# Optimization experiments

Measured on AMD Instinct MI355X. Metric: run time of the kernel, lower is better.

## Reference

```python
import jax, jax.numpy as jnp
import numpy as np

SEQ, BATCH, INP = 20, 16384, 2
HID, EMB = 256, 64
TARGET_LEN = 30


def setup_inputs() -> dict:
    key = jax.random.key(0)
    ks = jax.random.split(key, 12)
    s = 0.1
    return {
        "x_input": jax.random.normal(ks[0], (SEQ, BATCH, INP), dtype=jnp.float32),
        # encoder embedding Linear(input_size -> emb_dim)
        "W_emb": jax.random.normal(ks[1], (EMB, INP), dtype=jnp.float32) * s,
        "b_emb": jax.random.normal(ks[2], (EMB,), dtype=jnp.float32) * s,
        # encoder LSTM (input EMB -> hidden HID), PyTorch gate order i,f,g,o; bias = b_ih + b_hh
        "W_ih_enc": jax.random.normal(ks[3], (4 * HID, EMB), dtype=jnp.float32) * s,
        "W_hh_enc": jax.random.normal(ks[4], (4 * HID, HID), dtype=jnp.float32) * s,
        "b_enc": jax.random.normal(ks[5], (4 * HID,), dtype=jnp.float32) * s,
        # decoder LSTM (input INP -> hidden HID)
        "W_ih_dec": jax.random.normal(ks[6], (4 * HID, INP), dtype=jnp.float32) * s,
        "W_hh_dec": jax.random.normal(ks[7], (4 * HID, HID), dtype=jnp.float32) * s,
        "b_dec": jax.random.normal(ks[8], (4 * HID,), dtype=jnp.float32) * s,
        # decoder output Linear(hidden -> input_size)
        "W_out": jax.random.normal(ks[9], (INP, HID), dtype=jnp.float32) * s,
        "b_out": jax.random.normal(ks[10], (INP,), dtype=jnp.float32) * s,
        "target_len": TARGET_LEN,
    }


def _lstm_cell(x, h, c, W_ih, W_hh, b):
    # x: [B, in], h/c: [B, H]; PyTorch gate order: input, forget, cell(g), output
    gates = x @ W_ih.T + h @ W_hh.T + b  # [B, 4H]
    i, f, g, o = jnp.split(gates, 4, axis=-1)
    c_new = jax.nn.sigmoid(f) * c + jax.nn.sigmoid(i) * jnp.tanh(g)
    h_new = jax.nn.sigmoid(o) * jnp.tanh(c_new)
    return h_new, c_new


def reference(x_input, W_emb, b_emb, W_ih_enc, W_hh_enc, b_enc,
              W_ih_dec, W_hh_dec, b_dec, W_out, b_out, target_len):
    B = x_input.shape[1]
    # --- encoder ---
    x_emb = x_input @ W_emb.T + b_emb  # [S, B, EMB]
    h0 = jnp.zeros((B, HID), dtype=x_input.dtype)
    c0 = jnp.zeros((B, HID), dtype=x_input.dtype)

    def enc_step(carry, xt):
        h, c = carry
        h, c = _lstm_cell(xt, h, c, W_ih_enc, W_hh_enc, b_enc)
        return (h, c), None

    (h_enc, c_enc), _ = jax.lax.scan(enc_step, (h0, c0), x_emb)

    dec_in0 = x_input[-1]  # [B, INP]

    def dec_step(carry, _):
        di, h, c = carry
        h, c = _lstm_cell(di, h, c, W_ih_dec, W_hh_dec, b_dec)
        out = h @ W_out.T + b_out  # [B, INP]
        return (out, h, c), out

    _, outputs = jax.lax.scan(dec_step, (dec_in0, h_enc, c_enc), None,
                              length=int(target_len))
    return outputs  # [target_len, B, INP]
```

## Files before the change

kernel.cpp:

```cpp
#include <hip/hip_runtime.h>


#define SEQ  20
#define TLEN 30

typedef _Float16 half8   __attribute__((ext_vector_type(8)));
typedef _Float16 half4   __attribute__((ext_vector_type(4)));
typedef float    floatx4 __attribute__((ext_vector_type(4)));

__device__ _Float16 g_w_enc[1024 * 288];
__device__ _Float16 g_w_dec0[1024 * 288];
__device__ _Float16 g_w_deff[1024 * 288];
__device__ _Float16 g_wout[512];

__global__ void prep_kernel(const float* __restrict__ W_emb,
                            const float* __restrict__ b_emb,
                            const float* __restrict__ W_ih_enc,
                            const float* __restrict__ W_hh_enc,
                            const float* __restrict__ b_enc,
                            const float* __restrict__ W_ih_dec,
                            const float* __restrict__ W_hh_dec,
                            const float* __restrict__ b_dec,
                            const float* __restrict__ W_out,
                            const float* __restrict__ b_out) {
    int gid = blockIdx.x * blockDim.x + threadIdx.x;
    int stride = gridDim.x * blockDim.x;
    for (int s = gid; s < 1024 * 288; s += stride) {
        int n = s / 288, k = s - n * 288;
        int g = n >> 8, c = (n >> 4) & 15, l16 = n & 15;
        int w = c >> 1, cc = c & 1;
        int i = cc * 4 + g;
        int kt = k >> 5, q = (k >> 3) & 3, j = k & 7;
        int dst = ((w * 9 + kt) * 8 + i) * 512 + q * 128 + l16 * 8 + j;
        float fe = 0.f, fd = 0.f, ff = 0.f;
        if (k < 256) {
            fe = W_hh_enc[n * 256 + k];
            fd = W_hh_dec[n * 256 + k];
            ff = fd + W_ih_dec[2 * n] * W_out[k]
                    + W_ih_dec[2 * n + 1] * W_out[256 + k];
        } else {
            int kp = k - 256;
            if (kp < 2) {
                fd = W_ih_dec[2 * n + kp];
                const float* wr = &W_ih_enc[n * 64];
                for (int e = 0; e < 64; e++) fe = fmaf(wr[e], W_emb[2 * e + kp], fe);
            } else if (kp == 2) {
                fd = b_dec[n];
                ff = b_dec[n] + W_ih_dec[2 * n] * b_out[0]
                              + W_ih_dec[2 * n + 1] * b_out[1];
                fe = b_enc[n];
                const float* wr = &W_ih_enc[n * 64];
                for (int e = 0; e < 64; e++) fe = fmaf(wr[e], b_emb[e], fe);
            }
        }
        g_w_enc[dst]  = (_Float16)fe;
        g_w_dec0[dst] = (_Float16)fd;
        g_w_deff[dst] = (_Float16)ff;
    }
    if (gid < 512) g_wout[gid] = (_Float16)W_out[gid];
}

__global__ __launch_bounds__(512, 2) void lstm_fused(
        const float* __restrict__ x_input,
        const float* __restrict__ b_out,
        float* __restrict__ out)
{
    __shared__ __align__(16) _Float16 h_pack[2][18432];
    __shared__ __align__(16) float    partial_lds[2][8 * 132];

    const int tid = threadIdx.x;
    const int w   = tid >> 6;
    const int L   = tid & 63;
    const int l16 = L & 15;
    const int q   = L >> 4;
    const long row0 = (long)blockIdx.x * 64;

    {
        int* hz = (int*)&h_pack[0][0];
        for (int idx = tid; idx < 18432; idx += 512) hz[idx] = 0;
    }
    __syncthreads();
    if (tid < 128) {
        int buf = tid >> 6, b = tid & 63;
        h_pack[buf][((b >> 4) * 9 + 8) * 512 + (b & 15) * 8 + 2] = (_Float16)1.f;
    }
    if (tid < 128) {
        int b = tid >> 1, jj = tid & 1;
        h_pack[0][((b >> 4) * 9 + 8) * 512 + (b & 15) * 8 + jj] =
            (_Float16)x_input[(row0 + b) * 2 + jj];
    }

    const float bo = b_out[tid & 1];
    const int aoff = q * 128 + l16 * 8;
    const _Float16* __restrict__ wenc_w  = &g_w_enc[w * 36864];
    const _Float16* __restrict__ wdec0_w = &g_w_dec0[w * 36864];
    const _Float16* __restrict__ wdeff_w = &g_w_deff[w * 36864];

    _Float16 wo[2][2][4];
#pragma unroll
    for (int jj = 0; jj < 2; jj++)
#pragma unroll
        for (int cc = 0; cc < 2; cc++)
#pragma unroll
            for (int r = 0; r < 4; r++)
                wo[jj][cc][r] = g_wout[jj * 256 + 32 * w + 16 * cc + 4 * q + r];

    floatx4 acc[8][4];
    float   c_st[4][2][4];
#pragma unroll
    for (int nt = 0; nt < 4; nt++)
#pragma unroll
        for (int cc = 0; cc < 2; cc++)
#pragma unroll
            for (int r = 0; r < 4; r++) c_st[nt][cc][r] = 0.f;

    __syncthreads();

    int cur = 0;
#pragma unroll 1
    for (int t = 0; t < SEQ + TLEN; t++) {
        const _Float16* __restrict__ Wb =
            (t < SEQ) ? wenc_w : (t == SEQ) ? wdec0_w : wdeff_w;
        const _Float16* __restrict__ hp = h_pack[cur];
        _Float16* __restrict__ hn = h_pack[cur ^ 1];

#pragma unroll
        for (int i = 0; i < 8; i++)
#pragma unroll
            for (int nt = 0; nt < 4; nt++) acc[i][nt] = (floatx4)(0.f);

#pragma unroll
        for (int kt = 0; kt < 9; kt++) {
            half8 B[4];
#pragma unroll
            for (int nt = 0; nt < 4; nt++)
                B[nt] = *(const half8*)&hp[(nt * 9 + kt) * 512 + aoff];
#pragma unroll
            for (int i = 0; i < 8; i++) {
                half8 Aw = *(const half8*)&Wb[(kt * 8 + i) * 512 + aoff];
#pragma unroll
                for (int nt = 0; nt < 4; nt++)
                    acc[i][nt] = __builtin_amdgcn_mfma_f32_16x16x32_f16(
                        Aw, B[nt], acc[i][nt], 0, 0, 0);
            }
        }

        float xval = 0.f;
        if (t < SEQ && tid < 128) {
            int srct = (t + 1 < SEQ) ? t + 1 : SEQ - 1;
            xval = x_input[(long)srct * 32768 + (row0 + (tid >> 1)) * 2 + (tid & 1)];
        }

        const bool dec = (t >= SEQ);
        float po[4][2];
#pragma unroll
        for (int nt = 0; nt < 4; nt++) { po[nt][0] = 0.f; po[nt][1] = 0.f; }

#pragma unroll
        for (int nt = 0; nt < 4; nt++)
#pragma unroll
            for (int cc = 0; cc < 2; cc++) {
                half4 hv4;
                float hvf[4];
#pragma unroll
                for (int r = 0; r < 4; r++) {
                    float ai = acc[cc * 4 + 0][nt][r];
                    float af = acc[cc * 4 + 1][nt][r];
                    float ag = fmaxf(acc[cc * 4 + 2][nt][r], -30.f);
                    float ao = acc[cc * 4 + 3][nt][r];
                    float eI = __expf(-ai);
                    float eG = __expf(-2.f * ag);
                    float eF = __expf(-af);
                    float ig = (1.f - eG) *
                        __builtin_amdgcn_rcpf((1.f + eI) * (1.f + eG));
                    float fs = __builtin_amdgcn_rcpf(1.f + eF);
                    float cn = fmaf(fs, c_st[nt][cc][r], ig);
                    c_st[nt][cc][r] = cn;
                    float cnc = fmaxf(cn, -30.f);
                    float eO = __expf(-ao);
                    float eC = __expf(-2.f * cnc);
                    float hv = (1.f - eC) *
                        __builtin_amdgcn_rcpf((1.f + eO) * (1.f + eC));
                    hvf[r] = hv;
                    hv4[r] = (_Float16)hv;
                }
                *(half4*)&hn[(nt * 9 + w) * 512 + (2 * cc + (q >> 1)) * 128 +
                             l16 * 8 + 4 * (q & 1)] = hv4;
                if (dec) {
#pragma unroll
                    for (int r = 0; r < 4; r++) {
                        po[nt][0] = fmaf(hvf[r], (float)wo[0][cc][r], po[nt][0]);
                        po[nt][1] = fmaf(hvf[r], (float)wo[1][cc][r], po[nt][1]);
                    }
                }
            }

        if (dec) {
#pragma unroll
            for (int nt = 0; nt < 4; nt++)
#pragma unroll
                for (int jj = 0; jj < 2; jj++) {
                    float s = po[nt][jj];
                    s += __shfl_xor(s, 16);
                    s += __shfl_xor(s, 32);
                    po[nt][jj] = s;
                }
            if (q == 0) {
                float* pl = &partial_lds[t & 1][w * 132];
#pragma unroll
                for (int nt = 0; nt < 4; nt++) {
                    pl[nt * 16 + l16]      = po[nt][0];
                    pl[66 + nt * 16 + l16] = po[nt][1];
                }
            }
        }

        if (t < SEQ && tid < 128) {
            int b = tid >> 1, jj = tid & 1;
            hn[((b >> 4) * 9 + 8) * 512 + (b & 15) * 8 + jj] = (_Float16)xval;
        }

        __syncthreads();

        if (dec && tid < 128) {
            int m = tid >> 1, jj = tid & 1;
            const float* pl = &partial_lds[t & 1][jj * 66 + m];
            float s = bo;
#pragma unroll
            for (int w8 = 0; w8 < 8; w8++) s += pl[w8 * 132];
            out[(long)(t - SEQ) * 32768 + (row0 + m) * 2 + jj] = s;
        }

        cur ^= 1;
    }
}

extern "C" void kernel_launch(void* const* d_in, const int* in_sizes, int n_in,
                              void* d_out, int out_size, void* d_ws, size_t ws_size,
                              hipStream_t stream) {
    (void)in_sizes; (void)n_in; (void)d_ws; (void)ws_size; (void)out_size;
    const float* x      = (const float*)d_in[0];
    const float* W_emb  = (const float*)d_in[1];
    const float* b_emb  = (const float*)d_in[2];
    const float* W_ih_e = (const float*)d_in[3];
    const float* W_hh_e = (const float*)d_in[4];
    const float* b_enc  = (const float*)d_in[5];
    const float* W_ih_d = (const float*)d_in[6];
    const float* W_hh_d = (const float*)d_in[7];
    const float* b_dec  = (const float*)d_in[8];
    const float* W_out  = (const float*)d_in[9];
    const float* b_out  = (const float*)d_in[10];
    float* outp = (float*)d_out;

    prep_kernel<<<512, 256, 0, stream>>>(W_emb, b_emb, W_ih_e, W_hh_e, b_enc,
                                         W_ih_d, W_hh_d, b_dec, W_out, b_out);
    lstm_fused<<<256, 512, 0, stream>>>(x, b_out, outp);
}
```

Measured before the change: 660.3 us.

## Pre-scale gate weights by log2e, use exp2, stage last K-tile weights in LDS

```diff
diff --git a/kernel.cpp b/kernel.cpp
--- a/kernel.cpp
+++ b/kernel.cpp
@@ -3,6 +3,8 @@
 
 #define SEQ  20
 #define TLEN 30
+#define LOG2E  1.442695041f
+#define LOG2E2 2.885390082f
 
 typedef _Float16 half8   __attribute__((ext_vector_type(8)));
 typedef _Float16 half4   __attribute__((ext_vector_type(4)));
@@ -32,6 +34,7 @@
         int i = cc * 4 + g;
         int kt = k >> 5, q = (k >> 3) & 3, j = k & 7;
         int dst = ((w * 9 + kt) * 8 + i) * 512 + q * 128 + l16 * 8 + j;
+        float sc = (g == 2) ? LOG2E2 : LOG2E;
         float fe = 0.f, fd = 0.f, ff = 0.f;
         if (k < 256) {
             fe = W_hh_enc[n * 256 + k];
@@ -53,9 +56,9 @@
                 for (int e = 0; e < 64; e++) fe = fmaf(wr[e], b_emb[e], fe);
             }
         }
-        g_w_enc[dst]  = (_Float16)fe;
-        g_w_dec0[dst] = (_Float16)fd;
-        g_w_deff[dst] = (_Float16)ff;
+        g_w_enc[dst]  = (_Float16)(fe * sc);
+        g_w_dec0[dst] = (_Float16)(fd * sc);
+        g_w_deff[dst] = (_Float16)(ff * sc);
     }
     if (gid < 512) g_wout[gid] = (_Float16)W_out[gid];
 }
@@ -66,6 +69,7 @@
         float* __restrict__ out)
 {
     __shared__ __align__(16) _Float16 h_pack[2][18432];
+    __shared__ __align__(16) _Float16 w8_lds[8 * 4096];
     __shared__ __align__(16) float    partial_lds[2][8 * 132];
 
     const int tid = threadIdx.x;
@@ -75,9 +79,18 @@
     const int q   = L >> 4;
     const long row0 = (long)blockIdx.x * 64;
 
+    auto stage_w8 = [&](const _Float16* __restrict__ gsrc) {
+        int4* dst = (int4*)w8_lds;
+        for (int i4 = tid; i4 < 4096; i4 += 512) {
+            int wv = i4 >> 9, rest = i4 & 511;
+            dst[i4] = *(const int4*)&gsrc[(wv * 9 + 8) * 4096 + rest * 8];
+        }
+    };
+
     {
         int* hz = (int*)&h_pack[0][0];
         for (int idx = tid; idx < 18432; idx += 512) hz[idx] = 0;
+        stage_w8(g_w_enc);
     }
     __syncthreads();
     if (tid < 128) {
@@ -125,11 +138,6 @@
         _Float16* __restrict__ hn = h_pack[cur ^ 1];
 
 #pragma unroll
-        for (int i = 0; i < 8; i++)
-#pragma unroll
-            for (int nt = 0; nt < 4; nt++) acc[i][nt] = (floatx4)(0.f);
-
-#pragma unroll
         for (int kt = 0; kt < 9; kt++) {
             half8 B[4];
 #pragma unroll
@@ -137,11 +145,20 @@
                 B[nt] = *(const half8*)&hp[(nt * 9 + kt) * 512 + aoff];
 #pragma unroll
             for (int i = 0; i < 8; i++) {
-                half8 Aw = *(const half8*)&Wb[(kt * 8 + i) * 512 + aoff];
-#pragma unroll
-                for (int nt = 0; nt < 4; nt++)
-                    acc[i][nt] = __builtin_amdgcn_mfma_f32_16x16x32_f16(
-                        Aw, B[nt], acc[i][nt], 0, 0, 0);
+                half8 Aw = (kt < 8)
+                    ? *(const half8*)&Wb[(kt * 8 + i) * 512 + aoff]
+                    : *(const half8*)&w8_lds[w * 4096 + i * 512 + aoff];
+                if (kt == 0) {
+#pragma unroll
+                    for (int nt = 0; nt < 4; nt++)
+                        acc[i][nt] = __builtin_amdgcn_mfma_f32_16x16x32_f16(
+                            Aw, B[nt], (floatx4)(0.f), 0, 0, 0);
+                } else {
+#pragma unroll
+                    for (int nt = 0; nt < 4; nt++)
+                        acc[i][nt] = __builtin_amdgcn_mfma_f32_16x16x32_f16(
+                            Aw, B[nt], acc[i][nt], 0, 0, 0);
+                }
             }
         }
 
@@ -166,19 +183,19 @@
                 for (int r = 0; r < 4; r++) {
                     float ai = acc[cc * 4 + 0][nt][r];
                     float af = acc[cc * 4 + 1][nt][r];
-                    float ag = fmaxf(acc[cc * 4 + 2][nt][r], -30.f);
+                    float ag = acc[cc * 4 + 2][nt][r];
                     float ao = acc[cc * 4 + 3][nt][r];
-                    float eI = __expf(-ai);
-                    float eG = __expf(-2.f * ag);
-                    float eF = __expf(-af);
+                    float eI = __builtin_amdgcn_exp2f(-ai);
+                    float eG = __builtin_amdgcn_exp2f(-ag);
+                    float eF = __builtin_amdgcn_exp2f(-af);
+                    float eO = __builtin_amdgcn_exp2f(-ao);
                     float ig = (1.f - eG) *
                         __builtin_amdgcn_rcpf((1.f + eI) * (1.f + eG));
                     float fs = __builtin_amdgcn_rcpf(1.f + eF);
                     float cn = fmaf(fs, c_st[nt][cc][r], ig);
                     c_st[nt][cc][r] = cn;
-                    float cnc = fmaxf(cn, -30.f);
-                    float eO = __expf(-ao);
-                    float eC = __expf(-2.f * cnc);
+                    float cnc = fminf(fmaxf(cn, -12.f), 12.f);
+                    float eC = __builtin_amdgcn_exp2f(-LOG2E2 * cnc);
                     float hv = (1.f - eC) *
                         __builtin_amdgcn_rcpf((1.f + eO) * (1.f + eC));
                     hvf[r] = hv;
@@ -221,6 +238,9 @@
         }
 
         __syncthreads();
+
+        if (t == SEQ - 1) { stage_w8(g_w_dec0); __syncthreads(); }
+        else if (t == SEQ) { stage_w8(g_w_deff); __syncthreads(); }
 
         if (dec && tid < 128) {
             int m = tid >> 1, jj = tid & 1;
```

Result: slower. 697.5 us (+5.6%).
